# Kernel optimization log

Hardware: AMD Instinct MI355X
Metric: run time of the kernel (lower is better)

## Reference

```python
import jax, jax.numpy as jnp
import numpy as np

D_HEAD = 64  # per-head dim 'd' from init_kwargs


def layer_norm(x, g, b, eps=1e-5):
    m = x.mean(-1, keepdims=True)
    v = x.var(-1, keepdims=True)  # biased var, matches torch LayerNorm
    return (x - m) / jnp.sqrt(v + eps) * g + b


def setup_inputs() -> dict:
    key = jax.random.key(0)
    ks = jax.random.split(key, 16)
    F = 512
    B, T, N = 2, 8, 1024
    s = 1.0 / np.sqrt(F)
    u = lambda k, shape: jax.random.uniform(k, shape, jnp.float32, -s, s)
    return {
        "x": jax.random.normal(ks[0], (B, T, N, F), jnp.float32),
        "Wq": u(ks[1], (F, F)), "bq": u(ks[2], (F,)),
        "Wk": u(ks[3], (F, F)), "bk": u(ks[4], (F,)),
        "Wv": u(ks[5], (F, F)), "bv": u(ks[6], (F,)),
        "ln_g": jnp.ones((F,), jnp.float32), "ln_b": jnp.zeros((F,), jnp.float32),
        "W1": u(ks[7], (F, F)), "b1": u(ks[8], (F,)),
        "W2": u(ks[9], (F, F)), "b2": u(ks[10], (F,)),
        "lnff_g": jnp.ones((F,), jnp.float32), "lnff_b": jnp.zeros((F,), jnp.float32),
    }


def reference(x, Wq, bq, Wk, bk, Wv, bv, ln_g, ln_b, W1, b1, W2, b2, lnff_g, lnff_b):
    B, T, N, F = x.shape
    h = F // D_HEAD
    # q/k/v projections
    q = x @ Wq + bq
    k = x @ Wk + bk
    v = x @ Wv + bv
    # split last dim into heads (split+cat(dim=0) in torch == head axis here)
    qh = q.reshape(B, T, N, h, D_HEAD)
    kh = k.reshape(B, T, N, h, D_HEAD)
    vh = v.reshape(B, T, N, h, D_HEAD)
    # attention over node axis N per (batch, time, head)
    A = jnp.einsum('btqhd,btkhd->bthqk', qh, kh) / jnp.sqrt(jnp.asarray(D_HEAD, x.dtype))
    A = jax.nn.softmax(A, axis=-1)
    o = jnp.einsum('bthqk,btkhd->btqhd', A, vh).reshape(B, T, N, F)
    # residual + LN
    val = layer_norm(o + x, ln_g, ln_b)
    # FFN + final LN
    ff = jax.nn.relu(val @ W1 + b1) @ W2 + b2
    return layer_norm(ff, lnff_g, lnff_b)
```

## Files before the change

kernel.cpp:

```cpp
#include <hip/hip_runtime.h>
#include <hip/hip_bf16.h>

using bf16 = __hip_bfloat16;
typedef unsigned int u32x4 __attribute__((ext_vector_type(4)));
typedef float f32x4 __attribute__((ext_vector_type(4)));
typedef __bf16 bf16x8 __attribute__((ext_vector_type(8)));

#define DEVI __device__ __forceinline__

DEVI f32x4 mfma16(u32x4 a, u32x4 b, f32x4 c) {
    return __builtin_amdgcn_mfma_f32_16x16x32_bf16(
        __builtin_bit_cast(bf16x8, a), __builtin_bit_cast(bf16x8, b), c, 0, 0, 0);
}

DEVI void gload16(const bf16* g, bf16* l) {
    __builtin_amdgcn_global_load_lds(
        (const __attribute__((address_space(1))) unsigned int*)g,
        (__attribute__((address_space(3))) unsigned int*)l,
        16, 0, 0);
}

struct bf8 { bf16 h[8]; };

DEVI u32x4 pack8(f32x4 lo, f32x4 hi) {
    bf8 t;
#pragma unroll
    for (int i = 0; i < 4; i++) {
        t.h[i] = __float2bfloat16(lo[i]);
        t.h[4 + i] = __float2bfloat16(hi[i]);
    }
    return __builtin_bit_cast(u32x4, t);
}

DEVI unsigned long long pk4(float a, float b, float c, float d) {
    union { unsigned long long u; bf16 h[4]; } t;
    t.h[0] = __float2bfloat16(a); t.h[1] = __float2bfloat16(b);
    t.h[2] = __float2bfloat16(c); t.h[3] = __float2bfloat16(d);
    return t.u;
}

DEVI unsigned trunc2(float a, float b) {
    return __builtin_amdgcn_perm(__builtin_bit_cast(unsigned, b),
                                 __builtin_bit_cast(unsigned, a), 0x07060302);
}

__global__ __launch_bounds__(256) void prep(
    const float* __restrict__ Wq, const float* __restrict__ Wk,
    const float* __restrict__ Wv, const float* __restrict__ W1,
    const float* __restrict__ W2, const float* __restrict__ x,
    bf16* __restrict__ WT, bf16* __restrict__ xb)
{
    int b = blockIdx.x;
    if (b < 5120) {
        int w = b >> 10;
        const float* src = (w == 0) ? Wq : (w == 1) ? Wk : (w == 2) ? Wv : (w == 3) ? W1 : W2;
        int idx = (b & 1023) * 256 + threadIdx.x;
        int n = idx >> 9, kk = idx & 511;
        WT[(size_t)w * 262144 + idx] = __float2bfloat16(src[kk * 512 + n]);
    } else {
        size_t i = ((size_t)(b - 5120) * 256 + threadIdx.x) * 8;
        f32x4 lo = *(const f32x4*)&x[i];
        f32x4 hi = *(const f32x4*)&x[i + 4];
        *(u32x4*)&xb[i] = pack8(lo, hi);
    }
}

#define GEMM_BODY(EPILOGUE)                                                          \
    __shared__ __align__(16) bf16 As[128 * 64];                                      \
    __shared__ __align__(16) bf16 Bs[128 * 64];                                      \
    const int tid = threadIdx.x;                                                     \
    const int lane = tid & 63, wave = tid >> 6;                                      \
    const int wm = (wave >> 1) * 64, wn = (wave & 1) * 64;                           \
    const int lm = lane & 15, lq = lane >> 4;                                        \
    const int cxor = (lm & 7) * 8;                                                   \
    const int srow = wave * 32 + (lane >> 3);                                        \
    const int scol = ((lane & 7) ^ (lane >> 3)) * 8;                                 \
    const bf16* Ag = A + (size_t)(bm + srow) * 512 + scol;                           \
    const bf16* Bg = Bt + (size_t)(bn + srow) * 512 + scol;                          \
    bf16* Al = &As[wave * 32 * 64];                                                  \
    bf16* Bl = &Bs[wave * 32 * 64];                                                  \
    f32x4 acc[4][4];                                                                 \
    _Pragma("unroll") for (int i = 0; i < 4; i++)                                    \
        _Pragma("unroll") for (int j = 0; j < 4; j++)                                \
            acc[i][j] = (f32x4){0.f, 0.f, 0.f, 0.f};                                 \
    for (int k0 = 0; k0 < 512; k0 += 64) {                                           \
        __syncthreads();                   \
        _Pragma("unroll") for (int p = 0; p < 4; p++) {                              \
            gload16(Ag + (size_t)p * 8 * 512 + k0, Al + p * 512);                    \
            gload16(Bg + (size_t)p * 8 * 512 + k0, Bl + p * 512);                    \
        }                                                                            \
        __syncthreads();                   \
        _Pragma("unroll") for (int h = 0; h < 2; h++) {                              \
            u32x4 af[4], bfr[4];                                                     \
            _Pragma("unroll") for (int i = 0; i < 4; i++)                            \
                af[i] = *(const u32x4*)&As[(wm + i * 16 + lm) * 64 + ((h * 32 + lq * 8) ^ cxor)]; \
            _Pragma("unroll") for (int j = 0; j < 4; j++)                            \
                bfr[j] = *(const u32x4*)&Bs[(wn + j * 16 + lm) * 64 + ((h * 32 + lq * 8) ^ cxor)]; \
            EPILOGUE##_MMA                                                           \
        }                                                                            \
    }

#define SWAPPED_MMA                                                                  \
    _Pragma("unroll") for (int i = 0; i < 4; i++)                                    \
        _Pragma("unroll") for (int j = 0; j < 4; j++)                                \
            acc[i][j] = mfma16(bfr[j], af[i], acc[i][j]);
#define NORMAL_MMA                                                                   \
    _Pragma("unroll") for (int i = 0; i < 4; i++)                                    \
        _Pragma("unroll") for (int j = 0; j < 4; j++)                                \
            acc[i][j] = mfma16(af[i], bfr[j], acc[i][j]);

__global__ __launch_bounds__(256) void gemm_qk(
    const bf16* __restrict__ A, const bf16* __restrict__ WT,
    const float* __restrict__ bqp, const float* __restrict__ bkp,
    bf16* __restrict__ qb, bf16* __restrict__ kb)
{
    const int wsel = blockIdx.y >> 2;
    const int bm = blockIdx.x * 128, bn = (blockIdx.y & 3) * 128;
    const bf16* Bt = WT + (size_t)wsel * 262144;
    const float* bias = (wsel == 0) ? bqp : bkp;
    const float scale = (wsel == 0) ? 0.18033688f : 1.0f;
    bf16* dst = (wsel == 0) ? qb : kb;

    GEMM_BODY(SWAPPED)
#pragma unroll
    for (int i = 0; i < 4; i++) {
#pragma unroll
        for (int j = 0; j < 4; j++) {
            int row = bm + wm + i * 16 + lm;
            int colb = bn + wn + j * 16 + lq * 4;
            f32x4 b4 = *(const f32x4*)&bias[colb];
            *(unsigned long long*)&dst[(size_t)row * 512 + colb] =
                pk4((acc[i][j][0] + b4[0]) * scale, (acc[i][j][1] + b4[1]) * scale,
                    (acc[i][j][2] + b4[2]) * scale, (acc[i][j][3] + b4[3]) * scale);
        }
    }
}

__global__ __launch_bounds__(256) void gemm_v(
    const bf16* __restrict__ A, const bf16* __restrict__ WT,
    const float* __restrict__ bvp, bf16* __restrict__ vT)
{
    const int bm = blockIdx.x * 128, bn = blockIdx.y * 128;
    const bf16* Bt = WT + (size_t)2 * 262144;
    const float* bias = bvp;

    GEMM_BODY(NORMAL)
#pragma unroll
    for (int i = 0; i < 4; i++) {
#pragma unroll
        for (int j = 0; j < 4; j++) {
            int col = bn + wn + j * 16 + lm;
            float bv = bias[col];
            int rowb = bm + wm + i * 16 + lq * 4;
            int btq = rowb >> 10, node = rowb & 1023;
            int u = node & 31;
            int nodeP = (node & ~31) | (((u >> 2) & 3) << 3) | (((u >> 4) & 1) << 2);
            *(unsigned long long*)&vT[((size_t)((btq * 8 + (col >> 6)) * 64 + (col & 63))) * 1024 + nodeP] =
                pk4(acc[i][j][0] + bv, acc[i][j][1] + bv,
                    acc[i][j][2] + bv, acc[i][j][3] + bv);
        }
    }
}

template <bool RELU>
__global__ __launch_bounds__(256) void gemm_bt(
    const bf16* __restrict__ A, const bf16* __restrict__ Bt,
    const float* __restrict__ bias, bf16* __restrict__ C)
{
    const int bm = blockIdx.x * 128, bn = blockIdx.y * 128;
    GEMM_BODY(SWAPPED)
#pragma unroll
    for (int i = 0; i < 4; i++) {
#pragma unroll
        for (int j = 0; j < 4; j++) {
            int row = bm + wm + i * 16 + lm;
            int colb = bn + wn + j * 16 + lq * 4;
            f32x4 b4 = *(const f32x4*)&bias[colb];
            float c0 = acc[i][j][0] + b4[0], c1 = acc[i][j][1] + b4[1];
            float c2 = acc[i][j][2] + b4[2], c3 = acc[i][j][3] + b4[3];
            if (RELU) {
                c0 = fmaxf(c0, 0.f); c1 = fmaxf(c1, 0.f);
                c2 = fmaxf(c2, 0.f); c3 = fmaxf(c3, 0.f);
            }
            *(unsigned long long*)&C[(size_t)row * 512 + colb] = pk4(c0, c1, c2, c3);
        }
    }
}

__global__ __launch_bounds__(256, 4) void attn_kernel(
    const bf16* __restrict__ q, const bf16* __restrict__ k,
    const bf16* __restrict__ vT, float* __restrict__ o)
{
    constexpr int KP = 72;
    constexpr int VP = 72;
    __shared__ __align__(16) bf16 Ks[2][64 * KP];
    __shared__ __align__(16) bf16 Vs[2][64 * VP];

    const int tid = threadIdx.x, lane = tid & 63, wave = tid >> 6;
    const int group = blockIdx.x;
    const int bt = group >> 3, hh = group & 7;
    const int lm = lane & 15, lq = lane >> 4;
    const int qrow0 = bt * 1024 + blockIdx.y * 128 + wave * 32;

    u32x4 qf[2][2];
#pragma unroll
    for (int tm = 0; tm < 2; tm++)
#pragma unroll
        for (int kk2 = 0; kk2 < 2; kk2++)
            qf[tm][kk2] = *(const u32x4*)&q[(size_t)(qrow0 + tm * 16 + lm) * 512 + hh * 64 + kk2 * 32 + lq * 8];

    const bf16* kbase = k + (size_t)(bt * 1024) * 512 + hh * 64;
    const bf16* vbase = vT + (size_t)group * 64 * 1024;

    const int r0 = tid >> 3, e0 = (tid & 7) * 8;
    const int r1 = (256 + tid) >> 3;

    const unsigned ow = (lm == 0) ? 0x3F803F80u : 0u;
    const u32x4 onesA = (u32x4){ow, ow, ow, ow};

    f32x4 accO[4][2];
#pragma unroll
    for (int md = 0; md < 4; md++)
#pragma unroll
        for (int tm = 0; tm < 2; tm++) accO[md][tm] = (f32x4){0.f, 0.f, 0.f, 0.f};
    f32x4 accL[2] = {(f32x4){0.f, 0.f, 0.f, 0.f}, (f32x4){0.f, 0.f, 0.f, 0.f}};

    u32x4 kreg0 = *(const u32x4*)&kbase[(size_t)r0 * 512 + e0];
    u32x4 kreg1 = *(const u32x4*)&kbase[(size_t)r1 * 512 + e0];
    u32x4 vreg0 = *(const u32x4*)&vbase[(size_t)r0 * 1024 + e0];
    u32x4 vreg1 = *(const u32x4*)&vbase[(size_t)r1 * 1024 + e0];

    for (int kt = 0; kt < 16; kt++) {
        bf16* Kb = Ks[kt & 1];
        bf16* Vb = Vs[kt & 1];
        *(u32x4*)&Kb[r0 * KP + e0] = kreg0;
        *(u32x4*)&Kb[r1 * KP + e0] = kreg1;
        *(u32x4*)&Vb[r0 * VP + e0] = vreg0;
        *(u32x4*)&Vb[r1 * VP + e0] = vreg1;
        __syncthreads();
        if (kt < 15) {
            const bf16* kn = kbase + (size_t)((kt + 1) * 64) * 512;
            const bf16* vn = vbase + (kt + 1) * 64;
            kreg0 = *(const u32x4*)&kn[(size_t)r0 * 512 + e0];
            kreg1 = *(const u32x4*)&kn[(size_t)r1 * 512 + e0];
            vreg0 = *(const u32x4*)&vn[(size_t)r0 * 1024 + e0];
            vreg1 = *(const u32x4*)&vn[(size_t)r1 * 1024 + e0];
        }

#pragma unroll
        for (int kc = 0; kc < 2; kc++) {
            const int t0 = kc * 2;
            u32x4 kf00 = *(const u32x4*)&Kb[(t0 * 16 + lm) * KP + lq * 8];
            u32x4 kf01 = *(const u32x4*)&Kb[(t0 * 16 + lm) * KP + 32 + lq * 8];
            u32x4 kf10 = *(const u32x4*)&Kb[((t0 + 1) * 16 + lm) * KP + lq * 8];
            u32x4 kf11 = *(const u32x4*)&Kb[((t0 + 1) * 16 + lm) * KP + 32 + lq * 8];
            u32x4 pw[2];
#pragma unroll
            for (int tm = 0; tm < 2; tm++) {
                f32x4 s0 = (f32x4){0.f, 0.f, 0.f, 0.f};
                s0 = mfma16(kf00, qf[tm][0], s0);
                s0 = mfma16(kf01, qf[tm][1], s0);
                f32x4 s1 = (f32x4){0.f, 0.f, 0.f, 0.f};
                s1 = mfma16(kf10, qf[tm][0], s1);
                s1 = mfma16(kf11, qf[tm][1], s1);
                float p0 = __builtin_amdgcn_exp2f(s0[0]);
                float p1 = __builtin_amdgcn_exp2f(s0[1]);
                float p2 = __builtin_amdgcn_exp2f(s0[2]);
                float p3 = __builtin_amdgcn_exp2f(s0[3]);
                float p4 = __builtin_amdgcn_exp2f(s1[0]);
                float p5 = __builtin_amdgcn_exp2f(s1[1]);
                float p6 = __builtin_amdgcn_exp2f(s1[2]);
                float p7 = __builtin_amdgcn_exp2f(s1[3]);
                pw[tm] = (u32x4){trunc2(p0, p1), trunc2(p2, p3),
                                 trunc2(p4, p5), trunc2(p6, p7)};
            }
            accL[0] = mfma16(onesA, pw[0], accL[0]);
            accL[1] = mfma16(onesA, pw[1], accL[1]);
            __builtin_amdgcn_s_setprio(1);
#pragma unroll
            for (int md = 0; md < 4; md++) {
                u32x4 vf = *(const u32x4*)&Vb[(md * 16 + lm) * VP + kc * 32 + lq * 8];
                accO[md][0] = mfma16(vf, pw[0], accO[md][0]);
                accO[md][1] = mfma16(vf, pw[1], accO[md][1]);
            }
            __builtin_amdgcn_s_setprio(0);
        }
    }

#pragma unroll
    for (int tm = 0; tm < 2; tm++) {
        float l = accL[tm][0];
        l += __shfl_xor(l, 16);
        l += __shfl_xor(l, 32);
        float linv = 1.0f / l;
#pragma unroll
        for (int md = 0; md < 4; md++) {
            f32x4 r;
#pragma unroll
            for (int i = 0; i < 4; i++) r[i] = accO[md][tm][i] * linv;
            *(f32x4*)&o[(size_t)(qrow0 + tm * 16 + lm) * 512 + hh * 64 + md * 16 + lq * 4] = r;
        }
    }
}

template <bool AF32, bool RES, bool OF32>
__global__ __launch_bounds__(256) void ln_kernel(
    const void* __restrict__ a, const float* __restrict__ res,
    const float* __restrict__ g, const float* __restrict__ bb, void* __restrict__ out)
{
    int row = blockIdx.x * 4 + (threadIdx.x >> 6);
    int lane = threadIdx.x & 63;
    size_t base = (size_t)row * 512 + lane * 8;
    int cbase = lane * 8;

    float x8[8];
    if (AF32) {
        const float* af = (const float*)a;
        f32x4 lo = *(const f32x4*)&af[base];
        f32x4 hi = *(const f32x4*)&af[base + 4];
#pragma unroll
        for (int i = 0; i < 4; i++) { x8[i] = lo[i]; x8[4 + i] = hi[i]; }
    } else {
        bf8 av = __builtin_bit_cast(bf8, *(const u32x4*)&((const bf16*)a)[base]);
#pragma unroll
        for (int i = 0; i < 8; i++) x8[i] = __bfloat162float(av.h[i]);
    }
    if (RES) {
        f32x4 lo = *(const f32x4*)&res[base];
        f32x4 hi = *(const f32x4*)&res[base + 4];
#pragma unroll
        for (int i = 0; i < 4; i++) { x8[i] += lo[i]; x8[4 + i] += hi[i]; }
    }

    float s = 0.f, s2 = 0.f;
#pragma unroll
    for (int i = 0; i < 8; i++) { s += x8[i]; s2 += x8[i] * x8[i]; }
#pragma unroll
    for (int off = 1; off < 64; off <<= 1) {
        s += __shfl_xor(s, off);
        s2 += __shfl_xor(s2, off);
    }
    float mean = s * (1.f / 512.f);
    float var = s2 * (1.f / 512.f) - mean * mean;
    float rstd = rsqrtf(var + 1e-5f);

    f32x4 g0 = *(const f32x4*)&g[cbase], g1 = *(const f32x4*)&g[cbase + 4];
    f32x4 b0 = *(const f32x4*)&bb[cbase], b1v = *(const f32x4*)&bb[cbase + 4];
    float y[8];
#pragma unroll
    for (int i = 0; i < 4; i++) {
        y[i] = (x8[i] - mean) * rstd * g0[i] + b0[i];
        y[4 + i] = (x8[4 + i] - mean) * rstd * g1[i] + b1v[i];
    }
    if (OF32) {
        float* op = (float*)out;
        *(f32x4*)&op[base] = (f32x4){y[0], y[1], y[2], y[3]};
        *(f32x4*)&op[base + 4] = (f32x4){y[4], y[5], y[6], y[7]};
    } else {
        bf8 ov;
#pragma unroll
        for (int i = 0; i < 8; i++) ov.h[i] = __float2bfloat16(y[i]);
        *(u32x4*)&((bf16*)out)[base] = __builtin_bit_cast(u32x4, ov);
    }
}

extern "C" void kernel_launch(void* const* d_in, const int* in_sizes, int n_in,
                              void* d_out, int out_size, void* d_ws, size_t ws_size,
                              hipStream_t stream)
{
    const float* x    = (const float*)d_in[0];
    const float* Wq   = (const float*)d_in[1];
    const float* bq   = (const float*)d_in[2];
    const float* Wk   = (const float*)d_in[3];
    const float* bk   = (const float*)d_in[4];
    const float* Wv   = (const float*)d_in[5];
    const float* bv   = (const float*)d_in[6];
    const float* ln_g = (const float*)d_in[7];
    const float* ln_b = (const float*)d_in[8];
    const float* W1   = (const float*)d_in[9];
    const float* b1   = (const float*)d_in[10];
    const float* W2   = (const float*)d_in[11];
    const float* b2   = (const float*)d_in[12];
    const float* lnffg = (const float*)d_in[13];
    const float* lnffb = (const float*)d_in[14];
    float* out = (float*)d_out;

    bf16* ws = (bf16*)d_ws;
    bf16* WT = ws;
    bf16* qb = ws + 5 * 262144;
    bf16* kb = qb + 8388608;
    bf16* vT = kb + 8388608;
    bf16* vl = qb;
    bf16* f1 = kb;
    bf16* f2 = vT;
    bf16* xb = (bf16*)d_out;

    prep<<<9216, 256, 0, stream>>>(Wq, Wk, Wv, W1, W2, x, WT, xb);

    gemm_qk<<<dim3(128, 8), 256, 0, stream>>>(xb, WT, bq, bk, qb, kb);
    gemm_v <<<dim3(128, 4), 256, 0, stream>>>(xb, WT, bv, vT);

    attn_kernel<<<dim3(128, 8), 256, 0, stream>>>(qb, kb, vT, out);

    ln_kernel<true, true, false><<<4096, 256, 0, stream>>>(out, x, ln_g, ln_b, vl);

    dim3 gg(128, 4);
    gemm_bt<true> <<<gg, 256, 0, stream>>>(vl, WT + 3 * 262144, b1, f1);
    gemm_bt<false><<<gg, 256, 0, stream>>>(f1, WT + 4 * 262144, b2, f2);

    ln_kernel<false, false, true><<<4096, 256, 0, stream>>>(f2, nullptr, lnffg, lnffb, out);
}
```

Measured before the change: 245.9 us.

## Double-buffer LDS tiles in V-projection and FFN GEMMs

Adds a double-buffered variant of the shared-memory GEMM main loop. The next 64-wide K slice is loaded into the alternate LDS buffer before the MFMA work on the current buffer, so the global-to-LDS transfer overlaps with compute. The loop needs one barrier per step instead of two. The V-projection and FFN GEMMs use the new variant, while the QK GEMM keeps the single-buffered loop. This doubles the LDS use per block, which may lower the number of resident blocks per CU.

```diff
diff --git a/kernel.cpp b/kernel.cpp
--- a/kernel.cpp
+++ b/kernel.cpp
@@ -65,9 +65,7 @@
     }
 }
 
-#define GEMM_BODY(EPILOGUE)                                                          \
-    __shared__ __align__(16) bf16 As[128 * 64];                                      \
-    __shared__ __align__(16) bf16 Bs[128 * 64];                                      \
+#define GEMM_PROLOG                                                                  \
     const int tid = threadIdx.x;                                                     \
     const int lane = tid & 63, wave = tid >> 6;                                      \
     const int wm = (wave >> 1) * 64, wn = (wave & 1) * 64;                           \
@@ -77,17 +75,21 @@
     const int scol = ((lane & 7) ^ (lane >> 3)) * 8;                                 \
     const bf16* Ag = A + (size_t)(bm + srow) * 512 + scol;                           \
     const bf16* Bg = Bt + (size_t)(bn + srow) * 512 + scol;                          \
-    bf16* Al = &As[wave * 32 * 64];                                                  \
-    bf16* Bl = &Bs[wave * 32 * 64];                                                  \
+    const int lofs = wave * 32 * 64;                                                 \
     f32x4 acc[4][4];                                                                 \
     _Pragma("unroll") for (int i = 0; i < 4; i++)                                    \
         _Pragma("unroll") for (int j = 0; j < 4; j++)                                \
-            acc[i][j] = (f32x4){0.f, 0.f, 0.f, 0.f};                                 \
+            acc[i][j] = (f32x4){0.f, 0.f, 0.f, 0.f};
+
+#define GEMM_BODY(EPILOGUE)                                                          \
+    __shared__ __align__(16) bf16 As[128 * 64];                                      \
+    __shared__ __align__(16) bf16 Bs[128 * 64];                                      \
+    GEMM_PROLOG                                                                      \
     for (int k0 = 0; k0 < 512; k0 += 64) {                                           \
         __syncthreads();                   \
         _Pragma("unroll") for (int p = 0; p < 4; p++) {                              \
-            gload16(Ag + (size_t)p * 8 * 512 + k0, Al + p * 512);                    \
-            gload16(Bg + (size_t)p * 8 * 512 + k0, Bl + p * 512);                    \
+            gload16(Ag + (size_t)p * 8 * 512 + k0, &As[lofs + p * 512]);             \
+            gload16(Bg + (size_t)p * 8 * 512 + k0, &Bs[lofs + p * 512]);             \
         }                                                                            \
         __syncthreads();                   \
         _Pragma("unroll") for (int h = 0; h < 2; h++) {                              \
@@ -100,6 +102,33 @@
         }                                                                            \
     }
 
+#define GEMM_BODY_DB(EPILOGUE)                                                       \
+    __shared__ __align__(16) bf16 As[2][128 * 64];                                   \
+    __shared__ __align__(16) bf16 Bs[2][128 * 64];                                   \
+    GEMM_PROLOG                                                                      \
+    _Pragma("unroll") for (int p = 0; p < 4; p++) {                                  \
+        gload16(Ag + (size_t)p * 8 * 512, &As[0][lofs + p * 512]);                   \
+        gload16(Bg + (size_t)p * 8 * 512, &Bs[0][lofs + p * 512]);                   \
+    }                                                                                \
+    for (int k0 = 0; k0 < 512; k0 += 64) {                                           \
+        const int cur = (k0 >> 6) & 1;                                               \
+        __syncthreads();       \
+        if (k0 < 448) {          \
+            _Pragma("unroll") for (int p = 0; p < 4; p++) {                          \
+                gload16(Ag + (size_t)p * 8 * 512 + k0 + 64, &As[cur ^ 1][lofs + p * 512]); \
+                gload16(Bg + (size_t)p * 8 * 512 + k0 + 64, &Bs[cur ^ 1][lofs + p * 512]); \
+            }                                                                        \
+        }                                                                            \
+        _Pragma("unroll") for (int h = 0; h < 2; h++) {                              \
+            u32x4 af[4], bfr[4];                                                     \
+            _Pragma("unroll") for (int i = 0; i < 4; i++)                            \
+                af[i] = *(const u32x4*)&As[cur][(wm + i * 16 + lm) * 64 + ((h * 32 + lq * 8) ^ cxor)]; \
+            _Pragma("unroll") for (int j = 0; j < 4; j++)                            \
+                bfr[j] = *(const u32x4*)&Bs[cur][(wn + j * 16 + lm) * 64 + ((h * 32 + lq * 8) ^ cxor)]; \
+            EPILOGUE##_MMA                                                           \
+        }                                                                            \
+    }
+
 #define SWAPPED_MMA                                                                  \
     _Pragma("unroll") for (int i = 0; i < 4; i++)                                    \
         _Pragma("unroll") for (int j = 0; j < 4; j++)                                \
@@ -144,7 +173,7 @@
     const bf16* Bt = WT + (size_t)2 * 262144;
     const float* bias = bvp;
 
-    GEMM_BODY(NORMAL)
+    GEMM_BODY_DB(NORMAL)
 #pragma unroll
     for (int i = 0; i < 4; i++) {
 #pragma unroll
@@ -168,7 +197,7 @@
     const float* __restrict__ bias, bf16* __restrict__ C)
 {
     const int bm = blockIdx.x * 128, bn = blockIdx.y * 128;
-    GEMM_BODY(SWAPPED)
+    GEMM_BODY_DB(SWAPPED)
 #pragma unroll
     for (int i = 0; i < 4; i++) {
 #pragma unroll
```

Result: slower. 262.5 us (+6.7%).
